# Performance work log

Hardware: AMD Instinct MI355X
Metric: run time of the kernel (lower is better)

Reference implementation:

```python
import jax, jax.numpy as jnp
import numpy as np

B, K, C = 1024, 8, 10   # predicted points, concepts, classes per concept
N = 8192                # background (training) set size
EPS = 1e-13


def setup_inputs() -> dict:
    key = jax.random.key(0)
    k1, k2, k3 = jax.random.split(key, 3)
    c_p = jax.random.normal(k1, (B, K, C), dtype=jnp.float32)
    bandwidth = jnp.ones((K * C,), dtype=jnp.float32)  # learned param, init 1.0
    c_in = jax.random.randint(k2, (N, K), 0, C, dtype=jnp.int64)
    delta_in = jax.random.randint(k3, (N,), 0, 2, dtype=jnp.int32)
    return {"c_p": c_p, "bandwidth": bandwidth, "c_in": c_in, "delta_in": delta_in}


def _beran(c_p, bandwidth, c_in, delta_in):
    # ---- GaussKernel l2 metric ----
    proba = jax.nn.softmax(c_p, axis=-1)                      # [B,K,C]
    bw = jnp.clip(bandwidth, 0.001, 10.0).reshape(K, C)       # [K,C]
    onehot = jax.nn.one_hot(c_in, C, dtype=proba.dtype)       # [N,K,C]
    # sum((p - l)^2 / bw) = sum(p^2/bw) - 2 sum(p*l/bw) + sum(l^2/bw)
    A = jnp.sum(proba * proba / bw, axis=(1, 2))              # [B]
    D = jnp.einsum('nkc,kc->n', onehot, 1.0 / bw)             # [N]
    cross = jnp.einsum('bkc,nkc->bn', proba / bw, onehot)     # [B,N]
    metric = A[:, None] - 2.0 * cross + D[None, :]            # [B,N]
    weights = jnp.exp(-metric)
    s = jnp.sum(weights, axis=1, keepdims=True)               # normalize over background axis
    bad = s < EPS
    W = jnp.where(bad, 0.0, weights / jnp.where(bad, 1.0, s)) # [B,N]

    # ---- Beran cumulative hazard scan ----
    w_cumsum = jnp.cumsum(W, axis=1)
    shifted = w_cumsum - W
    ones = jnp.ones_like(shifted)
    bad2 = jnp.isclose(shifted, ones) | jnp.isclose(w_cumsum, ones)
    shifted = jnp.where(bad2, 0.0, shifted)
    w_cumsum = jnp.where(bad2, 0.0, w_cumsum)
    xi = jnp.log(1.0 - shifted) - jnp.log(1.0 - w_cumsum)
    filtered_xi = delta_in.astype(xi.dtype)[None, :] * xi
    hazards = jnp.cumsum(filtered_xi, axis=1)
    surv_func = jnp.exp(-hazards)                             # [B,N]
    first_step = 1.0 - surv_func[:, :1]
    surv_steps = jnp.concatenate([first_step, surv_func[:, :-1] - surv_func[:, 1:]], axis=1)
    ss = jnp.sum(surv_steps, axis=1, keepdims=True)
    bad3 = ss < EPS
    surv_steps = jnp.where(bad3, 0.0, surv_steps / jnp.where(bad3, 1.0, ss))
    return surv_func, surv_steps


def reference(c_p, bandwidth, c_in, delta_in):
    return _beran(c_p, bandwidth, c_in, delta_in)
```

## Files before the change

### kernel.cpp

```cpp
#include <hip/hip_runtime.h>

#define NN 8192
#define BB 1024
#define KK 8
#define CC 10
#define NT 512
#define CHUNK (NN/NT)
#define NW (NT/64)
#define T3SZ 2100
#define HALF 4096

typedef float f32x4 __attribute__((ext_vector_type(4)));

__device__ __forceinline__ int swz(int n) {
    return (n & ~31) | ((n + (n >> 5)) & 31);
}

__global__ void pack_kernel(const int* __restrict__ c_in, const int* __restrict__ delta_in,
                            unsigned* __restrict__ pairs, unsigned* __restrict__ dmask_g) {
    int n = blockIdx.x * blockDim.x + threadIdx.x;
    if (n >= NN) return;
    const int4* p = reinterpret_cast<const int4*>(c_in + (size_t)n * KK);
    int4 lo = p[0], hi = p[1];
    unsigned g0 = (unsigned)((lo.x * 10 + lo.y) * 10 + lo.z);
    unsigned g1 = (unsigned)((lo.w * 10 + hi.x) * 10 + hi.y);
    unsigned g2 = (unsigned)(hi.z * 10 + hi.w);
    pairs[n] = g0 | (g1 << 10) | (g2 << 20);
    unsigned long long bal = __ballot(delta_in[n] & 1);
    if ((threadIdx.x & 63) == 0) {
        dmask_g[n >> 5]       = (unsigned)(bal & 0xffffffffull);
        dmask_g[(n >> 5) + 1] = (unsigned)(bal >> 32);
    }
}

__global__ __launch_bounds__(NT, 8) void beran_kernel(
    const float* __restrict__ c_p, const float* __restrict__ bandwidth,
    const int* __restrict__ c_in, const int* __restrict__ delta_in,
    const unsigned* __restrict__ pairs, const unsigned* __restrict__ dmask_g,
    float* __restrict__ out)
{
    __shared__ float a2[HALF];
    __shared__ float tb[KK * CC];
    __shared__ float psc[KK * CC];
    __shared__ float t3[T3SZ];
    __shared__ float wsA[NW];
    __shared__ float wsM[NW];
    __shared__ float s4095;

    const int b    = blockIdx.x;
    const int t    = threadIdx.x;
    const int lane = t & 63;
    const int wv   = t >> 6;
    const int base = t * CHUNK;

    uint4 u0, u1, u2, u3;
    unsigned dm32 = 0;
    if (pairs) {
        const uint4* pp = reinterpret_cast<const uint4*>(pairs + base);
        u0 = pp[0]; u1 = pp[1]; u2 = pp[2]; u3 = pp[3];
        dm32 = dmask_g[t >> 1];
    }

    if (t < KK * CC) {
        const int k = t / CC, c = t - (t / CC) * CC;
        const float* row = c_p + ((size_t)b * KK + k) * CC;
        float mx = row[0];
        #pragma unroll
        for (int j = 1; j < CC; j++) mx = fmaxf(mx, row[j]);
        float se = 0.0f, ec = 0.0f;
        #pragma unroll
        for (int j = 0; j < CC; j++) {
            float e = __expf(row[j] - mx);
            se += e;
            if (j == c) ec = e;
        }
        float p  = ec * (1.0f / se);
        float bw = fminf(fmaxf(bandwidth[k * CC + c], 0.001f), 10.0f);
        float ib = 1.0f / bw;
        tb[t]  = ib - 2.0f * p * ib;
        psc[t] = p * p * ib;
    }
    __syncthreads();

    for (int i = t; i < T3SZ; i += NT) {
        float v;
        if (i < 1000) {
            v = tb[0*CC + i/100] + tb[1*CC + (i/10)%10] + tb[2*CC + i%10];
        } else if (i < 2000) {
            int j = i - 1000;
            v = tb[3*CC + j/100] + tb[4*CC + (j/10)%10] + tb[5*CC + j%10];
        } else {
            int q = i - 2000;
            float Ar = 0.0f;
            #pragma unroll
            for (int e = 0; e < KK * CC; e++) Ar += psc[e];
            v = tb[6*CC + q/10] + tb[7*CC + q%10] + Ar;
        }
        t3[i] = -v;
    }
    __syncthreads();

    float creg[CHUNK];
    unsigned dm = 0;
    float run = 0.0f;
    if (pairs) {
        dm = (dm32 >> ((t & 1) * 16)) & 0xffffu;
#define DO3(w0, idx) { \
        float m = t3[(w0) & 1023] + t3[1000 + (((w0) >> 10) & 1023)] \
                + t3[2000 + ((w0) >> 20)]; \
        run += __expf(m); creg[idx] = run; }
        DO3(u0.x,  0) DO3(u0.y,  1) DO3(u0.z,  2) DO3(u0.w,  3)
        DO3(u1.x,  4) DO3(u1.y,  5) DO3(u1.z,  6) DO3(u1.w,  7)
        DO3(u2.x,  8) DO3(u2.y,  9) DO3(u2.z, 10) DO3(u2.w, 11)
        DO3(u3.x, 12) DO3(u3.y, 13) DO3(u3.z, 14) DO3(u3.w, 15)
#undef DO3
    } else {
        float A = 0.0f;
        #pragma unroll
        for (int e = 0; e < KK * CC; e++) A += psc[e];
        #pragma unroll
        for (int i = 0; i < CHUNK; i++) {
            const int4* p4 = reinterpret_cast<const int4*>(c_in + (size_t)(base + i) * KK);
            int4 lo = p4[0], hi = p4[1];
            float m = A;
            m += tb[0*CC + lo.x] + tb[1*CC + lo.y] + tb[2*CC + lo.z] + tb[3*CC + lo.w];
            m += tb[4*CC + hi.x] + tb[5*CC + hi.y] + tb[6*CC + hi.z] + tb[7*CC + hi.w];
            run += __expf(-m);
            creg[i] = run;
            dm |= (unsigned)(delta_in[base + i] & 1) << i;
        }
    }

    float x = run;
    #pragma unroll
    for (int d = 1; d < 64; d <<= 1) {
        float y = __shfl_up(x, d);
        if (lane >= d) x += y;
    }
    if (lane == 63) wsA[wv] = x;
    __syncthreads();
    float s = 0.0f, woff = 0.0f;
    #pragma unroll
    for (int w = 0; w < NW; w++) {
        float y = wsA[w];
        s += y;
        if (w < wv) woff += y;
    }
    const float off_raw = woff + (x - run);
    const float invs = (s < 1e-13f) ? 0.0f : 1.0f / s;

    const float ISO = 1.00001e-5f;
    float uprev = 1.0f - off_raw * invs;
    float P = 1.0f;
    #pragma unroll
    for (int i = 0; i < CHUNK; i++) {
        float cs = (creg[i] + off_raw) * invs;
        float u  = 1.0f - cs;
        bool bad  = (fabsf(uprev) <= ISO) || (fabsf(u) <= ISO);
        bool flag = (dm >> i) & 1u;
        float f = (flag && !bad) ? u * __builtin_amdgcn_rcpf(uprev) : 1.0f;
        P *= f;
        creg[i] = P;
        uprev = u;
    }

    float xm = P;
    #pragma unroll
    for (int d = 1; d < 64; d <<= 1) {
        float y = __shfl_up(xm, d);
        if (lane >= d) xm *= y;
    }
    if (lane == 63) wsM[wv] = xm;
    __syncthreads();
    float tot = 1.0f, moff = 1.0f;
    #pragma unroll
    for (int w = 0; w < NW; w++) {
        float y = wsM[w];
        tot *= y;
        if (w < wv) moff *= y;
    }
    float exclm = __shfl_up(xm, 1);
    if (lane == 0) exclm = 1.0f;
    const float S_base = moff * exclm;

    #pragma unroll
    for (int i = 0; i < CHUNK; i++) creg[i] = S_base * creg[i];
    if (t == NT/2) s4095 = S_base;

    const float ss = 1.0f - tot;
    const float invss = (ss < 1e-13f) ? 0.0f : 1.0f / ss;
    float* outS = out + (size_t)b * NN;
    float* outT = out + (size_t)BB * NN + (size_t)b * NN;

    #pragma unroll
    for (int sidx = 0; sidx < 2; sidx++) {
        if ((t >> 8) == sidx) {
            const int lb = base - sidx * HALF;
            #pragma unroll
            for (int i = 0; i < CHUNK; i++) a2[swz(lb + i)] = creg[i];
        }
        __syncthreads();
        #pragma unroll
        for (int j = 0; j < 2; j++) {
            const int nl = j * 2048 + t * 4;
            const int n0 = sidx * HALF + nl;
            float s0 = a2[swz(nl)];
            float s1 = a2[swz(nl + 1)];
            float s2 = a2[swz(nl + 2)];
            float s3 = a2[swz(nl + 3)];
            float sp = (nl == 0) ? ((sidx == 0) ? 1.0f : s4095) : a2[swz(nl - 1)];
            f32x4 ov = {s0, s1, s2, s3};
            f32x4 st = {(sp - s0) * invss, (s0 - s1) * invss,
                        (s1 - s2) * invss, (s2 - s3) * invss};
            __builtin_nontemporal_store(ov, reinterpret_cast<f32x4*>(outS + n0));
            __builtin_nontemporal_store(st, reinterpret_cast<f32x4*>(outT + n0));
        }
        if (sidx == 0) __syncthreads();
    }
}

extern "C" void kernel_launch(void* const* d_in, const int* in_sizes, int n_in,
                              void* d_out, int out_size, void* d_ws, size_t ws_size,
                              hipStream_t stream) {
    const float* c_p       = (const float*)d_in[0];
    const float* bandwidth = (const float*)d_in[1];
    const int*   c_in      = (const int*)d_in[2];
    const int*   delta_in  = (const int*)d_in[3];
    float* out = (float*)d_out;

    unsigned* pairs   = nullptr;
    unsigned* dmask_g = nullptr;
    const size_t need = (size_t)NN * sizeof(unsigned) + (size_t)(NN / 32) * sizeof(unsigned);
    if (ws_size >= need) {
        pairs   = (unsigned*)d_ws;
        dmask_g = (unsigned*)((char*)d_ws + (size_t)NN * sizeof(unsigned));
        pack_kernel<<<NN / 256, 256, 0, stream>>>(c_in, delta_in, pairs, dmask_g);
    }
    beran_kernel<<<BB, NT, 0, stream>>>(c_p, bandwidth, c_in, delta_in, pairs, dmask_g, out);
}
```

Measured before the change: 28.69 us.

## Process two batch rows per 1024-thread block with full-row shared staging

Each block now uses 1024 threads, 8 elements per thread, and handles two batch rows in sequence. The softmax and lookup-table setup for both rows is done once per block before the per-row scans run. The whole 8192-element survival row is staged in shared memory at once, replacing the two-half staging pass and the s4095 handoff. Output stores change from nontemporal to regular vector stores. This cuts per-block setup and barrier overhead. In exchange, shared-memory use rises, the two rows run serially within a block, and __launch_bounds__(1024, 8) may squeeze registers.

New measurement: 38.04 us. 32.6% more time.

```diff
diff --git a/kernel.cpp b/kernel.cpp
--- a/kernel.cpp
+++ b/kernel.cpp
@@ -4,11 +4,12 @@
 #define BB 1024
 #define KK 8
 #define CC 10
-#define NT 512
+#define NT 1024
+#define ROWS 2
+#define GRID (BB/ROWS)
 #define CHUNK (NN/NT)
 #define NW (NT/64)
 #define T3SZ 2100
-#define HALF 4096
 
 typedef float f32x4 __attribute__((ext_vector_type(4)));
 
@@ -39,30 +40,35 @@
     const unsigned* __restrict__ pairs, const unsigned* __restrict__ dmask_g,
     float* __restrict__ out)
 {
-    __shared__ float a2[HALF];
-    __shared__ float tb[KK * CC];
-    __shared__ float psc[KK * CC];
-    __shared__ float t3[T3SZ];
-    __shared__ float wsA[NW];
-    __shared__ float wsM[NW];
-    __shared__ float s4095;
-
-    const int b    = blockIdx.x;
+    __shared__ float a[NN];
+    __shared__ float tb[ROWS][KK * CC];
+    __shared__ float psc[ROWS][KK * CC];
+    __shared__ float t3[ROWS][T3SZ];
+    __shared__ float wsA[ROWS][NW];
+    __shared__ float wsM[ROWS][NW];
+
     const int t    = threadIdx.x;
     const int lane = t & 63;
     const int wv   = t >> 6;
     const int base = t * CHUNK;
 
-    uint4 u0, u1, u2, u3;
-    unsigned dm32 = 0;
+    uint4 u0, u1;
+    unsigned dm = 0;
     if (pairs) {
         const uint4* pp = reinterpret_cast<const uint4*>(pairs + base);
-        u0 = pp[0]; u1 = pp[1]; u2 = pp[2]; u3 = pp[3];
-        dm32 = dmask_g[t >> 1];
-    }
-
-    if (t < KK * CC) {
-        const int k = t / CC, c = t - (t / CC) * CC;
+        u0 = pp[0]; u1 = pp[1];
+        dm = (dmask_g[t >> 2] >> ((t & 3) * 8)) & 0xffu;
+    } else {
+        #pragma unroll
+        for (int i = 0; i < CHUNK; i++)
+            dm |= (unsigned)(delta_in[base + i] & 1) << i;
+    }
+
+    if (t < ROWS * KK * CC) {
+        const int r = t / (KK * CC);
+        const int kc = t - r * (KK * CC);
+        const int k = kc / CC, c = kc - (kc / CC) * CC;
+        const int b = blockIdx.x * ROWS + r;
         const float* row = c_p + ((size_t)b * KK + k) * CC;
         float mx = row[0];
         #pragma unroll
@@ -75,147 +81,139 @@
             if (j == c) ec = e;
         }
         float p  = ec * (1.0f / se);
-        float bw = fminf(fmaxf(bandwidth[k * CC + c], 0.001f), 10.0f);
+        float bw = fminf(fmaxf(bandwidth[kc], 0.001f), 10.0f);
         float ib = 1.0f / bw;
-        tb[t]  = ib - 2.0f * p * ib;
-        psc[t] = p * p * ib;
+        tb[r][kc]  = ib - 2.0f * p * ib;
+        psc[r][kc] = p * p * ib;
     }
     __syncthreads();
 
-    for (int i = t; i < T3SZ; i += NT) {
+    for (int e = t; e < ROWS * T3SZ; e += NT) {
+        const int r = e / T3SZ;
+        const int i = e - r * T3SZ;
         float v;
         if (i < 1000) {
-            v = tb[0*CC + i/100] + tb[1*CC + (i/10)%10] + tb[2*CC + i%10];
+            v = tb[r][0*CC + i/100] + tb[r][1*CC + (i/10)%10] + tb[r][2*CC + i%10];
         } else if (i < 2000) {
             int j = i - 1000;
-            v = tb[3*CC + j/100] + tb[4*CC + (j/10)%10] + tb[5*CC + j%10];
+            v = tb[r][3*CC + j/100] + tb[r][4*CC + (j/10)%10] + tb[r][5*CC + j%10];
         } else {
             int q = i - 2000;
             float Ar = 0.0f;
             #pragma unroll
-            for (int e = 0; e < KK * CC; e++) Ar += psc[e];
-            v = tb[6*CC + q/10] + tb[7*CC + q%10] + Ar;
-        }
-        t3[i] = -v;
+            for (int e2 = 0; e2 < KK * CC; e2++) Ar += psc[r][e2];
+            v = tb[r][6*CC + q/10] + tb[r][7*CC + q%10] + Ar;
+        }
+        t3[r][i] = -v;
     }
     __syncthreads();
 
-    float creg[CHUNK];
-    unsigned dm = 0;
-    float run = 0.0f;
-    if (pairs) {
-        dm = (dm32 >> ((t & 1) * 16)) & 0xffffu;
+    #pragma unroll
+    for (int r = 0; r < ROWS; r++) {
+        const float* t3r = t3[r];
+        const int b = blockIdx.x * ROWS + r;
+
+        float creg[CHUNK];
+        float run = 0.0f;
+        if (pairs) {
 #define DO3(w0, idx) { \
-        float m = t3[(w0) & 1023] + t3[1000 + (((w0) >> 10) & 1023)] \
-                + t3[2000 + ((w0) >> 20)]; \
-        run += __expf(m); creg[idx] = run; }
-        DO3(u0.x,  0) DO3(u0.y,  1) DO3(u0.z,  2) DO3(u0.w,  3)
-        DO3(u1.x,  4) DO3(u1.y,  5) DO3(u1.z,  6) DO3(u1.w,  7)
-        DO3(u2.x,  8) DO3(u2.y,  9) DO3(u2.z, 10) DO3(u2.w, 11)
-        DO3(u3.x, 12) DO3(u3.y, 13) DO3(u3.z, 14) DO3(u3.w, 15)
+            float m = t3r[(w0) & 1023] + t3r[1000 + (((w0) >> 10) & 1023)] \
+                    + t3r[2000 + ((w0) >> 20)]; \
+            run += __expf(m); creg[idx] = run; }
+            DO3(u0.x, 0) DO3(u0.y, 1) DO3(u0.z, 2) DO3(u0.w, 3)
+            DO3(u1.x, 4) DO3(u1.y, 5) DO3(u1.z, 6) DO3(u1.w, 7)
 #undef DO3
-    } else {
-        float A = 0.0f;
-        #pragma unroll
-        for (int e = 0; e < KK * CC; e++) A += psc[e];
+        } else {
+            float A = 0.0f;
+            #pragma unroll
+            for (int e2 = 0; e2 < KK * CC; e2++) A += psc[r][e2];
+            #pragma unroll
+            for (int i = 0; i < CHUNK; i++) {
+                const int4* p4 = reinterpret_cast<const int4*>(c_in + (size_t)(base + i) * KK);
+                int4 lo = p4[0], hi = p4[1];
+                float m = A;
+                m += tb[r][0*CC + lo.x] + tb[r][1*CC + lo.y] + tb[r][2*CC + lo.z] + tb[r][3*CC + lo.w];
+                m += tb[r][4*CC + hi.x] + tb[r][5*CC + hi.y] + tb[r][6*CC + hi.z] + tb[r][7*CC + hi.w];
+                run += __expf(-m);
+                creg[i] = run;
+            }
+        }
+
+        float x = run;
+        #pragma unroll
+        for (int d = 1; d < 64; d <<= 1) {
+            float y = __shfl_up(x, d);
+            if (lane >= d) x += y;
+        }
+        if (lane == 63) wsA[r][wv] = x;
+        __syncthreads();
+        float s = 0.0f, woff = 0.0f;
+        #pragma unroll
+        for (int w = 0; w < NW; w++) {
+            float y = wsA[r][w];
+            s += y;
+            if (w < wv) woff += y;
+        }
+        const float off_raw = woff + (x - run);
+        const float invs = (s < 1e-13f) ? 0.0f : 1.0f / s;
+
+        const float ISO = 1.00001e-5f;
+        float uprev = 1.0f - off_raw * invs;
+        float P = 1.0f;
         #pragma unroll
         for (int i = 0; i < CHUNK; i++) {
-            const int4* p4 = reinterpret_cast<const int4*>(c_in + (size_t)(base + i) * KK);
-            int4 lo = p4[0], hi = p4[1];
-            float m = A;
-            m += tb[0*CC + lo.x] + tb[1*CC + lo.y] + tb[2*CC + lo.z] + tb[3*CC + lo.w];
-            m += tb[4*CC + hi.x] + tb[5*CC + hi.y] + tb[6*CC + hi.z] + tb[7*CC + hi.w];
-            run += __expf(-m);
-            creg[i] = run;
-            dm |= (unsigned)(delta_in[base + i] & 1) << i;
-        }
-    }
-
-    float x = run;
-    #pragma unroll
-    for (int d = 1; d < 64; d <<= 1) {
-        float y = __shfl_up(x, d);
-        if (lane >= d) x += y;
-    }
-    if (lane == 63) wsA[wv] = x;
-    __syncthreads();
-    float s = 0.0f, woff = 0.0f;
-    #pragma unroll
-    for (int w = 0; w < NW; w++) {
-        float y = wsA[w];
-        s += y;
-        if (w < wv) woff += y;
-    }
-    const float off_raw = woff + (x - run);
-    const float invs = (s < 1e-13f) ? 0.0f : 1.0f / s;
-
-    const float ISO = 1.00001e-5f;
-    float uprev = 1.0f - off_raw * invs;
-    float P = 1.0f;
-    #pragma unroll
-    for (int i = 0; i < CHUNK; i++) {
-        float cs = (creg[i] + off_raw) * invs;
-        float u  = 1.0f - cs;
-        bool bad  = (fabsf(uprev) <= ISO) || (fabsf(u) <= ISO);
-        bool flag = (dm >> i) & 1u;
-        float f = (flag && !bad) ? u * __builtin_amdgcn_rcpf(uprev) : 1.0f;
-        P *= f;
-        creg[i] = P;
-        uprev = u;
-    }
-
-    float xm = P;
-    #pragma unroll
-    for (int d = 1; d < 64; d <<= 1) {
-        float y = __shfl_up(xm, d);
-        if (lane >= d) xm *= y;
-    }
-    if (lane == 63) wsM[wv] = xm;
-    __syncthreads();
-    float tot = 1.0f, moff = 1.0f;
-    #pragma unroll
-    for (int w = 0; w < NW; w++) {
-        float y = wsM[w];
-        tot *= y;
-        if (w < wv) moff *= y;
-    }
-    float exclm = __shfl_up(xm, 1);
-    if (lane == 0) exclm = 1.0f;
-    const float S_base = moff * exclm;
-
-    #pragma unroll
-    for (int i = 0; i < CHUNK; i++) creg[i] = S_base * creg[i];
-    if (t == NT/2) s4095 = S_base;
-
-    const float ss = 1.0f - tot;
-    const float invss = (ss < 1e-13f) ? 0.0f : 1.0f / ss;
-    float* outS = out + (size_t)b * NN;
-    float* outT = out + (size_t)BB * NN + (size_t)b * NN;
-
-    #pragma unroll
-    for (int sidx = 0; sidx < 2; sidx++) {
-        if ((t >> 8) == sidx) {
-            const int lb = base - sidx * HALF;
-            #pragma unroll
-            for (int i = 0; i < CHUNK; i++) a2[swz(lb + i)] = creg[i];
-        }
+            float cs = (creg[i] + off_raw) * invs;
+            float u  = 1.0f - cs;
+            bool bad  = (fabsf(uprev) <= ISO) || (fabsf(u) <= ISO);
+            bool flag = (dm >> i) & 1u;
+            float f = (flag && !bad) ? u * __builtin_amdgcn_rcpf(uprev) : 1.0f;
+            P *= f;
+            creg[i] = P;
+            uprev = u;
+        }
+
+        float xm = P;
+        #pragma unroll
+        for (int d = 1; d < 64; d <<= 1) {
+            float y = __shfl_up(xm, d);
+            if (lane >= d) xm *= y;
+        }
+        if (lane == 63) wsM[r][wv] = xm;
         __syncthreads();
+        float tot = 1.0f, moff = 1.0f;
+        #pragma unroll
+        for (int w = 0; w < NW; w++) {
+            float y = wsM[r][w];
+            tot *= y;
+            if (w < wv) moff *= y;
+        }
+        float exclm = __shfl_up(xm, 1);
+        if (lane == 0) exclm = 1.0f;
+        const float S_base = moff * exclm;
+
+        #pragma unroll
+        for (int i = 0; i < CHUNK; i++) a[swz(base + i)] = S_base * creg[i];
+
+        const float ss = 1.0f - tot;
+        const float invss = (ss < 1e-13f) ? 0.0f : 1.0f / ss;
+        __syncthreads();
+
+        float* outS = out + (size_t)b * NN;
+        float* outT = out + (size_t)BB * NN + (size_t)b * NN;
         #pragma unroll
         for (int j = 0; j < 2; j++) {
-            const int nl = j * 2048 + t * 4;
-            const int n0 = sidx * HALF + nl;
-            float s0 = a2[swz(nl)];
-            float s1 = a2[swz(nl + 1)];
-            float s2 = a2[swz(nl + 2)];
-            float s3 = a2[swz(nl + 3)];
-            float sp = (nl == 0) ? ((sidx == 0) ? 1.0f : s4095) : a2[swz(nl - 1)];
+            const int n0 = j * 4096 + t * 4;
+            float s0 = a[swz(n0)];
+            float s1 = a[swz(n0 + 1)];
+            float s2 = a[swz(n0 + 2)];
+            float s3 = a[swz(n0 + 3)];
+            float sp = (n0 == 0) ? 1.0f : a[swz(n0 - 1)];
             f32x4 ov = {s0, s1, s2, s3};
             f32x4 st = {(sp - s0) * invss, (s0 - s1) * invss,
                         (s1 - s2) * invss, (s2 - s3) * invss};
-            __builtin_nontemporal_store(ov, reinterpret_cast<f32x4*>(outS + n0));
-            __builtin_nontemporal_store(st, reinterpret_cast<f32x4*>(outT + n0));
-        }
-        if (sidx == 0) __syncthreads();
+            *reinterpret_cast<f32x4*>(outS + n0) = ov;
+            *reinterpret_cast<f32x4*>(outT + n0) = st;
+        }
     }
 }
 
@@ -236,5 +234,5 @@
         dmask_g = (unsigned*)((char*)d_ws + (size_t)NN * sizeof(unsigned));
         pack_kernel<<<NN / 256, 256, 0, stream>>>(c_in, delta_in, pairs, dmask_g);
     }
-    beran_kernel<<<BB, NT, 0, stream>>>(c_p, bandwidth, c_in, delta_in, pairs, dmask_g, out);
-}
+    beran_kernel<<<GRID, NT, 0, stream>>>(c_p, bandwidth, c_in, delta_in, pairs, dmask_g, out);
+}
```
